# Kernel tuning notes

Hardware: AMD Instinct MI355X
Metric: run time of the kernel (lower is better)

The kernel has to match this reference:

```python
import jax, jax.numpy as jnp
import numpy as np

N, C, E = 100000, 128, 600000
H = C // 2  # 64


def setup_inputs() -> dict:
    key = jax.random.key(0)
    k1, k2, k3, k4, k5, k6, k7, k8 = jax.random.split(key, 8)
    z_in = jax.random.normal(k1, (N, C), dtype=jnp.float32)
    z_out = jax.random.normal(k2, (N, C), dtype=jnp.float32)
    z_self = jax.random.normal(k3, (N, C), dtype=jnp.float32)
    edge_index = jax.random.randint(k4, (2, E), 0, N, dtype=jnp.int64)
    # MLP params: Linear(C, C//2) -> ELU -> (Dropout eval=no-op) -> Linear(C//2, 1)
    lim1 = 1.0 / np.sqrt(C)
    W1 = jax.random.uniform(k5, (C, H), minval=-lim1, maxval=lim1, dtype=jnp.float32)
    b1 = jax.random.uniform(k6, (H,), minval=-lim1, maxval=lim1, dtype=jnp.float32)
    lim2 = 1.0 / np.sqrt(H)
    W2 = jax.random.uniform(k7, (H, 1), minval=-lim2, maxval=lim2, dtype=jnp.float32)
    b2 = jax.random.uniform(k8, (1,), minval=-lim2, maxval=lim2, dtype=jnp.float32)
    return {"z_in": z_in, "z_out": z_out, "z_self": z_self,
            "edge_index": edge_index, "W1": W1, "b1": b1, "W2": W2, "b2": b2}


def reference(z_in, z_out, z_self, edge_index, W1, b1, W2, b2):
    v1 = z_out + z_self                       # [N, C]
    v2 = z_in + z_self                        # [N, C]
    value = v1[edge_index[0]] * v2[edge_index[1]]  # [E, C] gather + elementwise product
    h = jax.nn.elu(value @ W1 + b1)           # [E, H]; dropout is identity at eval
    logits = h @ W2 + b2                      # [E, 1]
    return jax.nn.sigmoid(logits)
```

## Files before the change

### kernel.cpp

```cpp
#include <hip/hip_runtime.h>
#include <hip/hip_bf16.h>

typedef __attribute__((ext_vector_type(8))) short short8;
typedef __attribute__((ext_vector_type(4))) float f32x4;

__device__ __forceinline__ unsigned short f2bf(float f) {
    unsigned u = __float_as_uint(f);
    u += 0x7fffu + ((u >> 16) & 1u);
    return (unsigned short)(u >> 16);
}

__device__ __forceinline__ unsigned bfmul_trunc(unsigned a, unsigned b) {
    float al = __uint_as_float(a << 16);
    float ah = __uint_as_float(a & 0xffff0000u);
    float bl = __uint_as_float(b << 16);
    float bh = __uint_as_float(b & 0xffff0000u);
    unsigned pl = __float_as_uint(al * bl);
    unsigned ph = __float_as_uint(ah * bh);
    return __builtin_amdgcn_perm(ph, pl, 0x07060302u);
}

__device__ __forceinline__ unsigned pack_trunc(float lo, float hi) {
    return __builtin_amdgcn_perm(__float_as_uint(hi), __float_as_uint(lo), 0x07060302u);
}

__global__ __launch_bounds__(256) void prep_kernel(
    const float4* __restrict__ zin, const float4* __restrict__ zout,
    const float4* __restrict__ zself,
    ushort4* __restrict__ v1b, ushort4* __restrict__ v2b, int n4)
{
    int i = blockIdx.x * 256 + threadIdx.x;
    if (i >= n4) return;
    float4 o = zout[i], s = zself[i], z = zin[i];
    ushort4 a, b;
    a.x = f2bf(o.x + s.x); a.y = f2bf(o.y + s.y);
    a.z = f2bf(o.z + s.z); a.w = f2bf(o.w + s.w);
    b.x = f2bf(z.x + s.x); b.y = f2bf(z.y + s.y);
    b.z = f2bf(z.z + s.z); b.w = f2bf(z.w + s.w);
    v1b[i] = a; v2b[i] = b;
}

template <bool FUSED>
__global__ __launch_bounds__(256) void edge_kernel(
    const unsigned short* __restrict__ v1b, const unsigned short* __restrict__ v2b,
    const float* __restrict__ zin, const float* __restrict__ zout,
    const float* __restrict__ zself,
    const int* __restrict__ idx,
    const float* __restrict__ W1, const float* __restrict__ b1,
    const float* __restrict__ W2, const float* __restrict__ b2,
    float* __restrict__ out, int E, int ntiles)
{
    const int wave = threadIdx.x >> 6;
    const int lane = threadIdx.x & 63;
    const int nn = lane & 15;
    const int q  = lane >> 4;

    short8 Bf[4][4];
#pragma unroll
    for (int kc = 0; kc < 4; kc++)
#pragma unroll
        for (int jt = 0; jt < 4; jt++) {
            short8 v;
#pragma unroll
            for (int t = 0; t < 8; t++)
                v[t] = (short)f2bf(W1[(kc * 32 + q * 8 + t) * 64 + jt * 16 + nn]);
            Bf[kc][jt] = v;
        }
    float bias1[4], w2v[4];
#pragma unroll
    for (int jt = 0; jt < 4; jt++) {
        bias1[jt] = b1[jt * 16 + nn];
        w2v[jt]   = W2[jt * 16 + nn];
    }
    const float b2v = b2[0];

    const int nwaves = gridDim.x * 4;
    for (int tile = blockIdx.x * 4 + wave; tile < ntiles; tile += nwaves) {
        const int ebase = tile * 16;
        const int ee  = min(ebase + nn, E - 1);
        const int src = idx[ee];
        const int dst = idx[E + ee];

        short8 Af[4];
        if (FUSED) {
            const uint4* p1 = (const uint4*)(v1b + (size_t)src * 128);
            const uint4* p2 = (const uint4*)(v2b + (size_t)dst * 128);
            uint4 a[4], b[4];
#pragma unroll
            for (int kc = 0; kc < 4; kc++) {
                a[kc] = p1[kc * 4 + q];
                b[kc] = p2[kc * 4 + q];
            }
#pragma unroll
            for (int kc = 0; kc < 4; kc++) {
                uint4 p;
                p.x = bfmul_trunc(a[kc].x, b[kc].x);
                p.y = bfmul_trunc(a[kc].y, b[kc].y);
                p.z = bfmul_trunc(a[kc].z, b[kc].z);
                p.w = bfmul_trunc(a[kc].w, b[kc].w);
                Af[kc] = __builtin_bit_cast(short8, p);
            }
        } else {
            const float* po  = zout  + (size_t)src * 128 + q * 8;
            const float* ps1 = zself + (size_t)src * 128 + q * 8;
            const float* pi  = zin   + (size_t)dst * 128 + q * 8;
            const float* ps2 = zself + (size_t)dst * 128 + q * 8;
#pragma unroll
            for (int kc = 0; kc < 4; kc++) {
                float4 oa = *(const float4*)(po  + kc * 32), ob = *(const float4*)(po  + kc * 32 + 4);
                float4 sa = *(const float4*)(ps1 + kc * 32), sb = *(const float4*)(ps1 + kc * 32 + 4);
                float4 ia = *(const float4*)(pi  + kc * 32), ib = *(const float4*)(pi  + kc * 32 + 4);
                float4 ta = *(const float4*)(ps2 + kc * 32), tb = *(const float4*)(ps2 + kc * 32 + 4);
                uint4 p;
                p.x = pack_trunc((oa.x + sa.x) * (ia.x + ta.x), (oa.y + sa.y) * (ia.y + ta.y));
                p.y = pack_trunc((oa.z + sa.z) * (ia.z + ta.z), (oa.w + sa.w) * (ia.w + ta.w));
                p.z = pack_trunc((ob.x + sb.x) * (ib.x + tb.x), (ob.y + sb.y) * (ib.y + tb.y));
                p.w = pack_trunc((ob.z + sb.z) * (ib.z + tb.z), (ob.w + sb.w) * (ib.w + tb.w));
                Af[kc] = __builtin_bit_cast(short8, p);
            }
        }

        f32x4 acc[4];
#pragma unroll
        for (int jt = 0; jt < 4; jt++) acc[jt] = (f32x4){0.f, 0.f, 0.f, 0.f};
#pragma unroll
        for (int kc = 0; kc < 4; kc++)
#pragma unroll
            for (int jt = 0; jt < 4; jt++)
                acc[jt] = __builtin_amdgcn_mfma_f32_16x16x32_bf16(
                    Af[kc], Bf[kc][jt], acc[jt], 0, 0, 0);

        float ps[4];
#pragma unroll
        for (int r = 0; r < 4; r++) {
            float s = 0.f;
#pragma unroll
            for (int jt = 0; jt < 4; jt++) {
                float h = acc[jt][r] + bias1[jt];
                h = (h > 0.f) ? h : (__expf(h) - 1.f);
                s += h * w2v[jt];
            }
            ps[r] = s;
        }
#pragma unroll
        for (int off = 1; off < 16; off <<= 1) {
#pragma unroll
            for (int r = 0; r < 4; r++)
                ps[r] += __shfl_xor(ps[r], off, 64);
        }
        if (nn == 0) {
#pragma unroll
            for (int r = 0; r < 4; r++) {
                int e = ebase + q * 4 + r;
                if (e < E) {
                    float x = ps[r] + b2v;
                    out[e] = 1.f / (1.f + __expf(-x));
                }
            }
        }
    }
}

extern "C" void kernel_launch(void* const* d_in, const int* in_sizes, int n_in,
                              void* d_out, int out_size, void* d_ws, size_t ws_size,
                              hipStream_t stream)
{
    const float* zin   = (const float*)d_in[0];
    const float* zout  = (const float*)d_in[1];
    const float* zself = (const float*)d_in[2];
    const int*   idx   = (const int*)d_in[3];
    const float* W1    = (const float*)d_in[4];
    const float* b1    = (const float*)d_in[5];
    const float* W2    = (const float*)d_in[6];
    const float* b2    = (const float*)d_in[7];
    float* out = (float*)d_out;

    const int NC = in_sizes[0];
    const int E  = in_sizes[3] / 2;
    const int ntiles = (E + 15) / 16;
    const size_t need = (size_t)NC * 4;

    if (ws_size >= need) {
        unsigned short* v1b = (unsigned short*)d_ws;
        unsigned short* v2b = v1b + NC;
        const int n4 = NC / 4;
        prep_kernel<<<(n4 + 255) / 256, 256, 0, stream>>>(
            (const float4*)zin, (const float4*)zout, (const float4*)zself,
            (ushort4*)v1b, (ushort4*)v2b, n4);
        edge_kernel<true><<<2048, 256, 0, stream>>>(
            v1b, v2b, zin, zout, zself, idx, W1, b1, W2, b2, out, E, ntiles);
    } else {
        edge_kernel<false><<<2048, 256, 0, stream>>>(
            nullptr, nullptr, zin, zout, zself, idx, W1, b1, W2, b2, out, E, ntiles);
    }
}
```

Before: 243.5 us.

## Software-pipeline edge gathers and stage W1 fragments in LDS

Adds a new edge kernel that prefetches the next tile's bf16 row gathers into registers while the current tile runs its MFMA and epilogue. The W1 B-fragments move from 64 per-thread registers into shared memory, built once per block, and the launch bounds now allow 4 blocks per SIMD. The grid is halved to 1024 blocks. The goal is to hide gather latency and raise occupancy, at the cost of extra LDS reads per tile and double-buffered gather registers.

```diff
diff --git a/kernel.cpp b/kernel.cpp
--- a/kernel.cpp
+++ b/kernel.cpp
@@ -40,9 +40,128 @@
     v1b[i] = a; v2b[i] = b;
 }
 
-template <bool FUSED>
-__global__ __launch_bounds__(256) void edge_kernel(
+__global__ __launch_bounds__(256, 4) void edge_pipe(
     const unsigned short* __restrict__ v1b, const unsigned short* __restrict__ v2b,
+    const int* __restrict__ idx,
+    const float* __restrict__ W1, const float* __restrict__ b1,
+    const float* __restrict__ W2, const float* __restrict__ b2,
+    float* __restrict__ out, int E, int ntiles)
+{
+    __shared__ __align__(16) unsigned short ldsW[16 * 64 * 8];
+
+    const int tid  = threadIdx.x;
+    const int wave = tid >> 6;
+    const int lane = tid & 63;
+    const int nn = lane & 15;
+    const int q  = lane >> 4;
+
+#pragma unroll
+    for (int i = 0; i < 4; i++) {
+        int p = tid * 4 + i;
+        int f = p >> 6, l = p & 63;
+        int kc = f >> 2, jt = f & 3, lq = (l >> 4) & 3, ln = l & 15;
+        const float* wp = W1 + (size_t)(kc * 32 + lq * 8) * 64 + jt * 16 + ln;
+        uint4 wv;
+        wv.x = (unsigned)f2bf(wp[0 * 64]) | ((unsigned)f2bf(wp[1 * 64]) << 16);
+        wv.y = (unsigned)f2bf(wp[2 * 64]) | ((unsigned)f2bf(wp[3 * 64]) << 16);
+        wv.z = (unsigned)f2bf(wp[4 * 64]) | ((unsigned)f2bf(wp[5 * 64]) << 16);
+        wv.w = (unsigned)f2bf(wp[6 * 64]) | ((unsigned)f2bf(wp[7 * 64]) << 16);
+        *(uint4*)&ldsW[p * 8] = wv;
+    }
+    __syncthreads();
+
+    float bias1[4], w2v[4];
+#pragma unroll
+    for (int jt = 0; jt < 4; jt++) {
+        bias1[jt] = b1[jt * 16 + nn];
+        w2v[jt]   = W2[jt * 16 + nn];
+    }
+    const float b2v = b2[0];
+
+    const int nwaves = gridDim.x * 4;
+    int tile = blockIdx.x * 4 + wave;
+    if (tile >= ntiles) return;
+
+    int ee  = min(tile * 16 + nn, E - 1);
+    int src = idx[ee];
+    int dst = idx[E + ee];
+    uint4 a[4], b[4];
+    {
+        const uint4* p1 = (const uint4*)(v1b + (size_t)src * 128);
+        const uint4* p2 = (const uint4*)(v2b + (size_t)dst * 128);
+#pragma unroll
+        for (int kc = 0; kc < 4; kc++) { a[kc] = p1[kc * 4 + q]; b[kc] = p2[kc * 4 + q]; }
+    }
+
+    for (; tile < ntiles; tile += nwaves) {
+        const int tn = tile + nwaves;
+        const int tt = (tn < ntiles) ? tn : tile;
+        const int een  = min(tt * 16 + nn, E - 1);
+        const int srcn = idx[een];
+        const int dstn = idx[E + een];
+
+        short8 Af[4];
+#pragma unroll
+        for (int kc = 0; kc < 4; kc++) {
+            uint4 p;
+            p.x = bfmul_trunc(a[kc].x, b[kc].x);
+            p.y = bfmul_trunc(a[kc].y, b[kc].y);
+            p.z = bfmul_trunc(a[kc].z, b[kc].z);
+            p.w = bfmul_trunc(a[kc].w, b[kc].w);
+            Af[kc] = __builtin_bit_cast(short8, p);
+        }
+
+        {
+            const uint4* p1 = (const uint4*)(v1b + (size_t)srcn * 128);
+            const uint4* p2 = (const uint4*)(v2b + (size_t)dstn * 128);
+#pragma unroll
+            for (int kc = 0; kc < 4; kc++) { a[kc] = p1[kc * 4 + q]; b[kc] = p2[kc * 4 + q]; }
+        }
+
+        f32x4 acc[4];
+#pragma unroll
+        for (int jt = 0; jt < 4; jt++) acc[jt] = (f32x4){0.f, 0.f, 0.f, 0.f};
+#pragma unroll
+        for (int kc = 0; kc < 4; kc++) {
+#pragma unroll
+            for (int jt = 0; jt < 4; jt++) {
+                short8 Bf = *(const short8*)&ldsW[((kc * 4 + jt) * 64 + lane) * 8];
+                acc[jt] = __builtin_amdgcn_mfma_f32_16x16x32_bf16(Af[kc], Bf, acc[jt], 0, 0, 0);
+            }
+        }
+
+        float ps[4];
+#pragma unroll
+        for (int r = 0; r < 4; r++) {
+            float s = 0.f;
+#pragma unroll
+            for (int jt = 0; jt < 4; jt++) {
+                float h = acc[jt][r] + bias1[jt];
+                h = (h > 0.f) ? h : (__expf(h) - 1.f);
+                s += h * w2v[jt];
+            }
+            ps[r] = s;
+        }
+#pragma unroll
+        for (int off = 1; off < 16; off <<= 1) {
+#pragma unroll
+            for (int r = 0; r < 4; r++)
+                ps[r] += __shfl_xor(ps[r], off, 64);
+        }
+        if (nn == 0) {
+#pragma unroll
+            for (int r = 0; r < 4; r++) {
+                int e = tile * 16 + q * 4 + r;
+                if (e < E) {
+                    float x = ps[r] + b2v;
+                    out[e] = 1.f / (1.f + __expf(-x));
+                }
+            }
+        }
+    }
+}
+
+__global__ __launch_bounds__(256) void edge_f32(
     const float* __restrict__ zin, const float* __restrict__ zout,
     const float* __restrict__ zself,
     const int* __restrict__ idx,
@@ -82,42 +201,22 @@
         const int dst = idx[E + ee];
 
         short8 Af[4];
-        if (FUSED) {
-            const uint4* p1 = (const uint4*)(v1b + (size_t)src * 128);
-            const uint4* p2 = (const uint4*)(v2b + (size_t)dst * 128);
-            uint4 a[4], b[4];
-#pragma unroll
-            for (int kc = 0; kc < 4; kc++) {
-                a[kc] = p1[kc * 4 + q];
-                b[kc] = p2[kc * 4 + q];
-            }
-#pragma unroll
-            for (int kc = 0; kc < 4; kc++) {
-                uint4 p;
-                p.x = bfmul_trunc(a[kc].x, b[kc].x);
-                p.y = bfmul_trunc(a[kc].y, b[kc].y);
-                p.z = bfmul_trunc(a[kc].z, b[kc].z);
-                p.w = bfmul_trunc(a[kc].w, b[kc].w);
-                Af[kc] = __builtin_bit_cast(short8, p);
-            }
-        } else {
-            const float* po  = zout  + (size_t)src * 128 + q * 8;
-            const float* ps1 = zself + (size_t)src * 128 + q * 8;
-            const float* pi  = zin   + (size_t)dst * 128 + q * 8;
-            const float* ps2 = zself + (size_t)dst * 128 + q * 8;
-#pragma unroll
-            for (int kc = 0; kc < 4; kc++) {
-                float4 oa = *(const float4*)(po  + kc * 32), ob = *(const float4*)(po  + kc * 32 + 4);
-                float4 sa = *(const float4*)(ps1 + kc * 32), sb = *(const float4*)(ps1 + kc * 32 + 4);
-                float4 ia = *(const float4*)(pi  + kc * 32), ib = *(const float4*)(pi  + kc * 32 + 4);
-                float4 ta = *(const float4*)(ps2 + kc * 32), tb = *(const float4*)(ps2 + kc * 32 + 4);
-                uint4 p;
-                p.x = pack_trunc((oa.x + sa.x) * (ia.x + ta.x), (oa.y + sa.y) * (ia.y + ta.y));
-                p.y = pack_trunc((oa.z + sa.z) * (ia.z + ta.z), (oa.w + sa.w) * (ia.w + ta.w));
-                p.z = pack_trunc((ob.x + sb.x) * (ib.x + tb.x), (ob.y + sb.y) * (ib.y + tb.y));
-                p.w = pack_trunc((ob.z + sb.z) * (ib.z + tb.z), (ob.w + sb.w) * (ib.w + tb.w));
-                Af[kc] = __builtin_bit_cast(short8, p);
-            }
+        const float* po  = zout  + (size_t)src * 128 + q * 8;
+        const float* ps1 = zself + (size_t)src * 128 + q * 8;
+        const float* pi  = zin   + (size_t)dst * 128 + q * 8;
+        const float* ps2 = zself + (size_t)dst * 128 + q * 8;
+#pragma unroll
+        for (int kc = 0; kc < 4; kc++) {
+            float4 oa = *(const float4*)(po  + kc * 32), ob = *(const float4*)(po  + kc * 32 + 4);
+            float4 sa = *(const float4*)(ps1 + kc * 32), sb = *(const float4*)(ps1 + kc * 32 + 4);
+            float4 ia = *(const float4*)(pi  + kc * 32), ib = *(const float4*)(pi  + kc * 32 + 4);
+            float4 ta = *(const float4*)(ps2 + kc * 32), tb = *(const float4*)(ps2 + kc * 32 + 4);
+            uint4 p;
+            p.x = pack_trunc((oa.x + sa.x) * (ia.x + ta.x), (oa.y + sa.y) * (ia.y + ta.y));
+            p.y = pack_trunc((oa.z + sa.z) * (ia.z + ta.z), (oa.w + sa.w) * (ia.w + ta.w));
+            p.z = pack_trunc((ob.x + sb.x) * (ib.x + tb.x), (ob.y + sb.y) * (ib.y + tb.y));
+            p.w = pack_trunc((ob.z + sb.z) * (ib.z + tb.z), (ob.w + sb.w) * (ib.w + tb.w));
+            Af[kc] = __builtin_bit_cast(short8, p);
         }
 
         f32x4 acc[4];
@@ -127,8 +226,7 @@
         for (int kc = 0; kc < 4; kc++)
 #pragma unroll
             for (int jt = 0; jt < 4; jt++)
-                acc[jt] = __builtin_amdgcn_mfma_f32_16x16x32_bf16(
-                    Af[kc], Bf[kc][jt], acc[jt], 0, 0, 0);
+                acc[jt] = __builtin_amdgcn_mfma_f32_16x16x32_bf16(Af[kc], Bf[kc][jt], acc[jt], 0, 0, 0);
 
         float ps[4];
 #pragma unroll
@@ -187,10 +285,10 @@
         prep_kernel<<<(n4 + 255) / 256, 256, 0, stream>>>(
             (const float4*)zin, (const float4*)zout, (const float4*)zself,
             (ushort4*)v1b, (ushort4*)v2b, n4);
-        edge_kernel<true><<<2048, 256, 0, stream>>>(
-            v1b, v2b, zin, zout, zself, idx, W1, b1, W2, b2, out, E, ntiles);
+        edge_pipe<<<1024, 256, 0, stream>>>(
+            v1b, v2b, idx, W1, b1, W2, b2, out, E, ntiles);
     } else {
-        edge_kernel<false><<<2048, 256, 0, stream>>>(
-            nullptr, nullptr, zin, zout, zself, idx, W1, b1, W2, b2, out, E, ntiles);
-    }
-}
+        edge_f32<<<2048, 256, 0, stream>>>(
+            zin, zout, zself, idx, W1, b1, W2, b2, out, E, ntiles);
+    }
+}
```

New measurement: 227.7 us. 6.5% less time.
